# Kernel tuning notes

Hardware: AMD Instinct MI355X
Metric: run time of the kernel (lower is better)

## Reference

```python
import jax, jax.numpy as jnp
import numpy as np

TOP_K = 2
LOGIT_SCALE = 1.0


def setup_inputs() -> dict:
    key = jax.random.key(0)
    k = jax.random.split(key, 5)
    B, S, C = 1, 1024, 1024
    E, I = 8, 1024           # experts, per-expert intermediate
    x = jax.random.normal(k[0], (B, S, C), dtype=jnp.float32)
    router_w = jax.random.normal(k[1], (E, C), dtype=jnp.float32) * 0.02
    w_in = jax.random.normal(k[2], (E, 2 * I, C), dtype=jnp.float32) * 0.02
    b_in = jnp.zeros((E, 2 * I), dtype=jnp.float32)
    w_out = jax.random.normal(k[3], (E, C, I), dtype=jnp.float32) * 0.02
    b_out = jnp.zeros((E, C), dtype=jnp.float32)
    return {"x": x, "router_w": router_w, "w_in": w_in, "b_in": b_in,
            "w_out": w_out, "b_out": b_out}


def reference(x, router_w, w_in, b_in, w_out, b_out):
    B, S, C = x.shape
    E = router_w.shape[0]
    xt = x.reshape(-1, C)                               # [T, C] flattened tokens
    T = xt.shape[0]

    # Router: softmax over all experts, then top-k probs as combine weights.
    logits = (xt @ router_w.T) * LOGIT_SCALE            # [T, E]
    probs = jax.nn.softmax(logits, axis=-1)
    top_w, top_idx = jax.lax.top_k(probs, TOP_K)        # [T, K]

    # Sparse gate matrix: nonzero only at the top-k experts per token.
    gate = jnp.zeros((T, E), dtype=probs.dtype)
    gate = gate.at[jnp.arange(T)[:, None], top_idx].set(top_w)  # [T, E]

    # Expert SwiGLU MLP, dense over experts, masked combine by gate.
    h = jnp.einsum('tc,eoc->teo', xt, w_in) + b_in      # [T, E, 2I]
    g, u = jnp.split(h, 2, axis=-1)                     # gate / input halves
    a = jax.nn.silu(g) * u                              # swiglu  [T, E, I]
    y = jnp.einsum('tei,eci->tec', a, w_out) + b_out    # [T, E, C]
    out = jnp.einsum('te,tec->tc', gate, y)             # combine top-k experts
    return out.reshape(B, S, C)
```

## Files before the change

kernel.cpp:

```cpp
#include <hip/hip_runtime.h>
#include <hip/hip_bf16.h>
#include <stdint.h>

#define TTOK 1024
#define CDIM 1024
#define NEXP 8
#define IDIM 1024
#define TWOI 2048
#define NSLOT 2048

typedef float f32x4 __attribute__((ext_vector_type(4)));
typedef short s16x8 __attribute__((ext_vector_type(8)));
typedef unsigned short u16;
typedef u16 u16x4 __attribute__((ext_vector_type(4)));
typedef u16 u16x8 __attribute__((ext_vector_type(8)));

__device__ __forceinline__ u16 f2bf(float f) {
  unsigned x = __float_as_uint(f);
  x += 0x7fffu + ((x >> 16) & 1u);
  return (u16)(x >> 16);
}

__device__ __forceinline__ void gload_lds16(const void* g, void* l) {
  __builtin_amdgcn_global_load_lds(
      (const __attribute__((address_space(1))) void*)g,
      (__attribute__((address_space(3))) void*)l, 16, 0, 0);
}

__global__ __launch_bounds__(64) void router_k(const float* __restrict__ x,
                                               const float* __restrict__ rw,
                                               float* __restrict__ topw,
                                               int* __restrict__ topidx,
                                               u16* __restrict__ xb) {
  const int t = blockIdx.x;
  const int lane = threadIdx.x;
  float p[NEXP];
#pragma unroll
  for (int e = 0; e < NEXP; ++e) p[e] = 0.f;
  const float* xr = x + (size_t)t * CDIM;
  u16* xbr = xb + (size_t)t * CDIM;
  for (int c0 = lane * 4; c0 < CDIM; c0 += 64 * 4) {
    f32x4 xv = *(const f32x4*)(xr + c0);
    u16x4 xc;
#pragma unroll
    for (int q = 0; q < 4; ++q) xc[q] = f2bf(xv[q]);
    *(u16x4*)(xbr + c0) = xc;
#pragma unroll
    for (int e = 0; e < NEXP; ++e) {
      f32x4 wv = *(const f32x4*)(rw + (size_t)e * CDIM + c0);
      p[e] += xv[0] * wv[0] + xv[1] * wv[1] + xv[2] * wv[2] + xv[3] * wv[3];
    }
  }
#pragma unroll
  for (int e = 0; e < NEXP; ++e) {
    float v = p[e];
#pragma unroll
    for (int off = 32; off >= 1; off >>= 1) v += __shfl_xor(v, off);
    p[e] = v;
  }
  if (lane == 0) {
    float m = p[0];
#pragma unroll
    for (int e = 1; e < NEXP; ++e) m = fmaxf(m, p[e]);
    float pe[NEXP];
    float den = 0.f;
#pragma unroll
    for (int e = 0; e < NEXP; ++e) { pe[e] = __expf(p[e] - m); den += pe[e]; }
    int i0 = 0;
#pragma unroll
    for (int e = 1; e < NEXP; ++e) if (p[e] > p[i0]) i0 = e;
    int i1 = (i0 == 0) ? 1 : 0;
#pragma unroll
    for (int e = 0; e < NEXP; ++e) if (e != i0 && p[e] > p[i1]) i1 = e;
    const float inv = 1.f / den;
    topw[t * 2] = pe[i0] * inv;
    topw[t * 2 + 1] = pe[i1] * inv;
    topidx[t * 2] = i0;
    topidx[t * 2 + 1] = i1;
  }
}

__global__ __launch_bounds__(1024) void build_k(const int* __restrict__ topidx,
                                                int* __restrict__ meta,
                                                int* __restrict__ slot_token,
                                                int* __restrict__ slot_expert,
                                                int* __restrict__ tok2slot) {
  __shared__ int cnt[NEXP], off[NEXP], cur[NEXP];
  const int t = threadIdx.x;
  if (t < NEXP) { cnt[t] = 0; cur[t] = 0; }
  __syncthreads();
  const int e0 = topidx[t * 2];
  const int e1 = topidx[t * 2 + 1];
  atomicAdd(&cnt[e0], 1);
  atomicAdd(&cnt[e1], 1);
  __syncthreads();
  if (t == 0) {
    int acc = 0;
    for (int e = 0; e < NEXP; ++e) { off[e] = acc; acc += cnt[e]; }
  }
  __syncthreads();
  if (t < NEXP) { meta[t] = cnt[t]; meta[16 + t] = off[t]; }
  {
    const int p0 = atomicAdd(&cur[e0], 1);
    const int s0 = off[e0] + p0;
    slot_token[s0] = t;
    slot_expert[s0] = e0;
    tok2slot[t * 2] = s0;
    const int p1 = atomicAdd(&cur[e1], 1);
    const int s1 = off[e1] + p1;
    slot_token[s1] = t;
    slot_expert[s1] = e1;
    tok2slot[t * 2 + 1] = s1;
  }
}

template <int BM, bool GATHER, bool BIAS>
__global__ __launch_bounds__(256) void gemm_k(const u16* __restrict__ A,
                                              const float* __restrict__ W,
                                              float* __restrict__ O,
                                              const float* __restrict__ bias,
                                              const int* __restrict__ meta,
                                              const int* __restrict__ slot_token,
                                              int N, int K) {
  constexpr int BN = 64;
  constexpr int WM = BM / 2;
  constexpr int WN = BN / 2;
  constexpr int MR = WM / 16;
  constexpr int NR = WN / 16;
  constexpr int AG = BM / 32;

  const int e = blockIdx.z;
  const int cnt = meta[e];
  const int m0 = blockIdx.y * BM;
  if (m0 >= cnt) return;
  const int off = meta[16 + e];
  const int n0 = blockIdx.x * BN;

  __shared__ u16 sA[2][BM * 64];
  __shared__ u16 sB[2][BN * 64];

  const int tid = threadIdx.x;
  const int lane = tid & 63;
  const int w = tid >> 6;
  const int wr = w >> 1;
  const int wc = w & 1;

  const u16* aSrc[AG];
#pragma unroll
  for (int i = 0; i < AG; ++i) {
    const int r = w * (BM / 4) + i * 8 + (lane >> 3);
    int rr = m0 + r;
    if (rr > cnt - 1) rr = cnt - 1;
    const int rowg = GATHER ? slot_token[off + rr] : (off + rr);
    const int cs = (lane & 7) ^ (r & 7);
    aSrc[i] = A + (size_t)rowg * K + cs * 8;
  }
  int aDst[AG];
#pragma unroll
  for (int i = 0; i < AG; ++i) aDst[i] = (w * (BM / 4) + i * 8) * 64 + lane * 8;

  const int brow = tid >> 2;
  const int bq = tid & 3;
  const float* bSrc = W + ((size_t)e * N + (n0 + brow)) * K + bq * 16;
  const int brow7 = brow & 7;
  const int bOff0 = brow * 64 + (((bq * 2) ^ brow7) * 8);
  const int bOff1 = brow * 64 + (((bq * 2 + 1) ^ brow7) * 8);

  f32x4 acc[MR][NR];
#pragma unroll
  for (int m = 0; m < MR; ++m)
#pragma unroll
    for (int n = 0; n < NR; ++n) acc[m][n] = (f32x4){0.f, 0.f, 0.f, 0.f};

  {
#pragma unroll
    for (int i = 0; i < AG; ++i) gload_lds16(aSrc[i], &sA[0][aDst[i]]);
    f32x4 v0 = *(const f32x4*)(bSrc);
    f32x4 v1 = *(const f32x4*)(bSrc + 4);
    f32x4 v2 = *(const f32x4*)(bSrc + 8);
    f32x4 v3 = *(const f32x4*)(bSrc + 12);
    u16x8 lo, hi;
#pragma unroll
    for (int q = 0; q < 4; ++q) lo[q] = f2bf(v0[q]);
#pragma unroll
    for (int q = 0; q < 4; ++q) lo[4 + q] = f2bf(v1[q]);
#pragma unroll
    for (int q = 0; q < 4; ++q) hi[q] = f2bf(v2[q]);
#pragma unroll
    for (int q = 0; q < 4; ++q) hi[4 + q] = f2bf(v3[q]);
    *(u16x8*)(&sB[0][bOff0]) = lo;
    *(u16x8*)(&sB[0][bOff1]) = hi;
  }
  __syncthreads();

  int c = 0;
  for (int k0 = 0; k0 < K; k0 += 64) {
    const int nk = k0 + 64;
    const bool has_next = nk < K;

    f32x4 v0, v1, v2, v3;
    if (has_next) {
#pragma unroll
      for (int i = 0; i < AG; ++i) gload_lds16(aSrc[i] + nk, &sA[1 - c][aDst[i]]);
      const float* bs = bSrc + nk;
      v0 = *(const f32x4*)(bs);
      v1 = *(const f32x4*)(bs + 4);
      v2 = *(const f32x4*)(bs + 8);
      v3 = *(const f32x4*)(bs + 12);
    }

#pragma unroll
    for (int kh = 0; kh < 2; ++kh) {
      const int j = kh * 4 + (lane >> 4);
      s16x8 af[MR], bf[NR];
#pragma unroll
      for (int m = 0; m < MR; ++m) {
        const int r = wr * WM + m * 16 + (lane & 15);
        af[m] = *(const s16x8*)(&sA[c][r * 64 + ((j ^ (r & 7)) * 8)]);
      }
#pragma unroll
      for (int n = 0; n < NR; ++n) {
        const int r = wc * WN + n * 16 + (lane & 15);
        bf[n] = *(const s16x8*)(&sB[c][r * 64 + ((j ^ (r & 7)) * 8)]);
      }
#pragma unroll
      for (int m = 0; m < MR; ++m)
#pragma unroll
        for (int n = 0; n < NR; ++n)
          acc[m][n] = __builtin_amdgcn_mfma_f32_16x16x32_bf16(af[m], bf[n], acc[m][n], 0, 0, 0);
    }

    if (has_next) {
      u16x8 lo, hi;
#pragma unroll
      for (int q = 0; q < 4; ++q) lo[q] = f2bf(v0[q]);
#pragma unroll
      for (int q = 0; q < 4; ++q) lo[4 + q] = f2bf(v1[q]);
#pragma unroll
      for (int q = 0; q < 4; ++q) hi[q] = f2bf(v2[q]);
#pragma unroll
      for (int q = 0; q < 4; ++q) hi[4 + q] = f2bf(v3[q]);
      *(u16x8*)(&sB[1 - c][bOff0]) = lo;
      *(u16x8*)(&sB[1 - c][bOff1]) = hi;
    }

    __syncthreads();
    c ^= 1;
  }

#pragma unroll
  for (int m = 0; m < MR; ++m) {
#pragma unroll
    for (int jj = 0; jj < 4; ++jj) {
      const int tr = wr * WM + m * 16 + ((lane >> 4) * 4) + jj;
      if (m0 + tr < cnt) {
        const size_t slot = (size_t)(off + m0 + tr);
#pragma unroll
        for (int n = 0; n < NR; ++n) {
          const int col = n0 + wc * WN + n * 16 + (lane & 15);
          float v = acc[m][n][jj];
          if (BIAS) v += bias[(size_t)e * N + col];
          O[slot * N + col] = v;
        }
      }
    }
  }
}

__global__ __launch_bounds__(256) void swiglu_k(const float* __restrict__ h,
                                                const float* __restrict__ b_in,
                                                const int* __restrict__ slot_expert,
                                                u16* __restrict__ a) {
  const int s = blockIdx.x;
  const int e = slot_expert[s];
  const int i = threadIdx.x * 4;
  f32x4 g = *(const f32x4*)(h + (size_t)s * TWOI + i);
  f32x4 u = *(const f32x4*)(h + (size_t)s * TWOI + IDIM + i);
  f32x4 bg = *(const f32x4*)(b_in + (size_t)e * TWOI + i);
  f32x4 bu = *(const f32x4*)(b_in + (size_t)e * TWOI + IDIM + i);
  u16x4 o;
#pragma unroll
  for (int q = 0; q < 4; ++q) {
    const float gg = g[q] + bg[q];
    const float uu = u[q] + bu[q];
    const float sv = gg / (1.f + __expf(-gg));
    o[q] = f2bf(sv * uu);
  }
  *(u16x4*)(a + (size_t)s * IDIM + i) = o;
}

__global__ __launch_bounds__(256) void combine_k(const float* __restrict__ y,
                                                 const float* __restrict__ topw,
                                                 const int* __restrict__ tok2slot,
                                                 float* __restrict__ out) {
  const int idx = blockIdx.x * 256 + threadIdx.x;
  const int t = idx >> 8;
  const int c4 = (idx & 255) * 4;
  const int s0 = tok2slot[t * 2];
  const int s1 = tok2slot[t * 2 + 1];
  const float w0 = topw[t * 2];
  const float w1 = topw[t * 2 + 1];
  f32x4 y0 = *(const f32x4*)(y + (size_t)s0 * CDIM + c4);
  f32x4 y1 = *(const f32x4*)(y + (size_t)s1 * CDIM + c4);
  f32x4 o;
#pragma unroll
  for (int q = 0; q < 4; ++q) o[q] = w0 * y0[q] + w1 * y1[q];
  *(f32x4*)(out + (size_t)t * CDIM + c4) = o;
}

extern "C" void kernel_launch(void* const* d_in, const int* in_sizes, int n_in,
                              void* d_out, int out_size, void* d_ws, size_t ws_size,
                              hipStream_t stream) {
  const float* x = (const float*)d_in[0];
  const float* rw = (const float*)d_in[1];
  const float* w_in = (const float*)d_in[2];
  const float* b_in = (const float*)d_in[3];
  const float* w_out = (const float*)d_in[4];
  const float* b_out = (const float*)d_in[5];
  float* out = (float*)d_out;
  char* ws = (char*)d_ws;

  int* meta = (int*)ws;
  int* slot_token = (int*)(ws + 1024);
  int* slot_expert = (int*)(ws + 1024 + 8192);
  int* tok2slot = (int*)(ws + 1024 + 16384);
  float* topw = (float*)(ws + 1024 + 24576);
  int* topidx = (int*)(ws + 1024 + 32768);
  u16* xb = (u16*)(ws + 65536);
  float* h = (float*)(ws + 65536 + (2u << 20));
  u16* a = (u16*)(ws + 65536 + (18u << 20));
  float* y = (float*)(ws + 65536 + (22u << 20));

  router_k<<<TTOK, 64, 0, stream>>>(x, rw, topw, topidx, xb);
  build_k<<<1, 1024, 0, stream>>>(topidx, meta, slot_token, slot_expert, tok2slot);
  gemm_k<128, true, false><<<dim3(32, 16, NEXP), 256, 0, stream>>>(
      xb, w_in, h, nullptr, meta, slot_token, TWOI, CDIM);
  swiglu_k<<<NSLOT, 256, 0, stream>>>(h, b_in, slot_expert, a);
  gemm_k<64, false, true><<<dim3(16, 32, NEXP), 256, 0, stream>>>(
      a, w_out, y, b_out, meta, slot_token, CDIM, IDIM);
  combine_k<<<1024, 256, 0, stream>>>(y, topw, tok2slot, out);
}
```

Before: 197.9 us.

## Fuse SwiGLU into first GEMM epilogue and combine into second via atomics

The first expert GEMM now interleaves gate and up rows of w_in so each tile holds matching g/u columns. It applies bias and SwiGLU in its epilogue via a lane shuffle and writes bf16 activations directly, which removes the fp32 h buffer and the separate swiglu kernel. The second GEMM scales by the gate weight and atomically adds into a zeroed output, which removes the y buffer and the combine kernel. In exchange it adds a memset, float atomics with nondeterministic summation order, and a smaller BM=64 tile for GEMM1 that rereads the weights more often.

```diff
diff --git a/kernel.cpp b/kernel.cpp
--- a/kernel.cpp
+++ b/kernel.cpp
@@ -81,10 +81,10 @@
 }
 
 __global__ __launch_bounds__(1024) void build_k(const int* __restrict__ topidx,
+                                                const float* __restrict__ topw,
                                                 int* __restrict__ meta,
                                                 int* __restrict__ slot_token,
-                                                int* __restrict__ slot_expert,
-                                                int* __restrict__ tok2slot) {
+                                                float* __restrict__ gatew) {
   __shared__ int cnt[NEXP], off[NEXP], cur[NEXP];
   const int t = threadIdx.x;
   if (t < NEXP) { cnt[t] = 0; cur[t] = 0; }
@@ -104,40 +104,30 @@
     const int p0 = atomicAdd(&cur[e0], 1);
     const int s0 = off[e0] + p0;
     slot_token[s0] = t;
-    slot_expert[s0] = e0;
-    tok2slot[t * 2] = s0;
+    gatew[s0] = topw[t * 2];
     const int p1 = atomicAdd(&cur[e1], 1);
     const int s1 = off[e1] + p1;
     slot_token[s1] = t;
-    slot_expert[s1] = e1;
-    tok2slot[t * 2 + 1] = s1;
-  }
-}
-
-template <int BM, bool GATHER, bool BIAS>
-__global__ __launch_bounds__(256) void gemm_k(const u16* __restrict__ A,
-                                              const float* __restrict__ W,
-                                              float* __restrict__ O,
-                                              const float* __restrict__ bias,
-                                              const int* __restrict__ meta,
-                                              const int* __restrict__ slot_token,
-                                              int N, int K) {
-  constexpr int BN = 64;
-  constexpr int WM = BM / 2;
-  constexpr int WN = BN / 2;
-  constexpr int MR = WM / 16;
-  constexpr int NR = WN / 16;
-  constexpr int AG = BM / 32;
-
+    gatew[s1] = topw[t * 2 + 1];
+  }
+}
+
+__global__ __launch_bounds__(256) void gemm1_k(const u16* __restrict__ A,
+                                               const float* __restrict__ W,
+                                               const float* __restrict__ b_in,
+                                               u16* __restrict__ Aout,
+                                               const int* __restrict__ meta,
+                                               const int* __restrict__ slot_token) {
+  constexpr int BM = 64, K = CDIM;
   const int e = blockIdx.z;
   const int cnt = meta[e];
   const int m0 = blockIdx.y * BM;
   if (m0 >= cnt) return;
   const int off = meta[16 + e];
-  const int n0 = blockIdx.x * BN;
+  const int i0 = blockIdx.x * 32;
 
   __shared__ u16 sA[2][BM * 64];
-  __shared__ u16 sB[2][BN * 64];
+  __shared__ u16 sB[2][64 * 64];
 
   const int tid = threadIdx.x;
   const int lane = tid & 63;
@@ -145,36 +135,36 @@
   const int wr = w >> 1;
   const int wc = w & 1;
 
-  const u16* aSrc[AG];
-#pragma unroll
-  for (int i = 0; i < AG; ++i) {
-    const int r = w * (BM / 4) + i * 8 + (lane >> 3);
+  const u16* aSrc[2];
+  int aDst[2];
+#pragma unroll
+  for (int i = 0; i < 2; ++i) {
+    const int r = w * 16 + i * 8 + (lane >> 3);
     int rr = m0 + r;
     if (rr > cnt - 1) rr = cnt - 1;
-    const int rowg = GATHER ? slot_token[off + rr] : (off + rr);
+    const int rowg = slot_token[off + rr];
     const int cs = (lane & 7) ^ (r & 7);
     aSrc[i] = A + (size_t)rowg * K + cs * 8;
-  }
-  int aDst[AG];
-#pragma unroll
-  for (int i = 0; i < AG; ++i) aDst[i] = (w * (BM / 4) + i * 8) * 64 + lane * 8;
+    aDst[i] = (w * 16 + i * 8) * 64 + lane * 8;
+  }
 
   const int brow = tid >> 2;
   const int bq = tid & 3;
-  const float* bSrc = W + ((size_t)e * N + (n0 + brow)) * K + bq * 16;
+  const int wrow = (brow & 1) ? (IDIM + i0 + (brow >> 1)) : (i0 + (brow >> 1));
+  const float* bSrc = W + ((size_t)e * TWOI + wrow) * K + bq * 16;
   const int brow7 = brow & 7;
   const int bOff0 = brow * 64 + (((bq * 2) ^ brow7) * 8);
   const int bOff1 = brow * 64 + (((bq * 2 + 1) ^ brow7) * 8);
 
-  f32x4 acc[MR][NR];
-#pragma unroll
-  for (int m = 0; m < MR; ++m)
-#pragma unroll
-    for (int n = 0; n < NR; ++n) acc[m][n] = (f32x4){0.f, 0.f, 0.f, 0.f};
+  f32x4 acc[2][2];
+#pragma unroll
+  for (int m = 0; m < 2; ++m)
+#pragma unroll
+    for (int n = 0; n < 2; ++n) acc[m][n] = (f32x4){0.f, 0.f, 0.f, 0.f};
 
   {
 #pragma unroll
-    for (int i = 0; i < AG; ++i) gload_lds16(aSrc[i], &sA[0][aDst[i]]);
+    for (int i = 0; i < 2; ++i) gload_lds16(aSrc[i], &sA[0][aDst[i]]);
     f32x4 v0 = *(const f32x4*)(bSrc);
     f32x4 v1 = *(const f32x4*)(bSrc + 4);
     f32x4 v2 = *(const f32x4*)(bSrc + 8);
@@ -197,39 +187,36 @@
   for (int k0 = 0; k0 < K; k0 += 64) {
     const int nk = k0 + 64;
     const bool has_next = nk < K;
-
     f32x4 v0, v1, v2, v3;
     if (has_next) {
 #pragma unroll
-      for (int i = 0; i < AG; ++i) gload_lds16(aSrc[i] + nk, &sA[1 - c][aDst[i]]);
+      for (int i = 0; i < 2; ++i) gload_lds16(aSrc[i] + nk, &sA[1 - c][aDst[i]]);
       const float* bs = bSrc + nk;
       v0 = *(const f32x4*)(bs);
       v1 = *(const f32x4*)(bs + 4);
       v2 = *(const f32x4*)(bs + 8);
       v3 = *(const f32x4*)(bs + 12);
     }
-
 #pragma unroll
     for (int kh = 0; kh < 2; ++kh) {
       const int j = kh * 4 + (lane >> 4);
-      s16x8 af[MR], bf[NR];
-#pragma unroll
-      for (int m = 0; m < MR; ++m) {
-        const int r = wr * WM + m * 16 + (lane & 15);
+      s16x8 af[2], bf[2];
+#pragma unroll
+      for (int m = 0; m < 2; ++m) {
+        const int r = wr * 32 + m * 16 + (lane & 15);
         af[m] = *(const s16x8*)(&sA[c][r * 64 + ((j ^ (r & 7)) * 8)]);
       }
 #pragma unroll
-      for (int n = 0; n < NR; ++n) {
-        const int r = wc * WN + n * 16 + (lane & 15);
+      for (int n = 0; n < 2; ++n) {
+        const int r = wc * 32 + n * 16 + (lane & 15);
         bf[n] = *(const s16x8*)(&sB[c][r * 64 + ((j ^ (r & 7)) * 8)]);
       }
 #pragma unroll
-      for (int m = 0; m < MR; ++m)
-#pragma unroll
-        for (int n = 0; n < NR; ++n)
+      for (int m = 0; m < 2; ++m)
+#pragma unroll
+        for (int n = 0; n < 2; ++n)
           acc[m][n] = __builtin_amdgcn_mfma_f32_16x16x32_bf16(af[m], bf[n], acc[m][n], 0, 0, 0);
     }
-
     if (has_next) {
       u16x8 lo, hi;
 #pragma unroll
@@ -243,69 +230,172 @@
       *(u16x8*)(&sB[1 - c][bOff0]) = lo;
       *(u16x8*)(&sB[1 - c][bOff1]) = hi;
     }
-
     __syncthreads();
     c ^= 1;
   }
 
 #pragma unroll
-  for (int m = 0; m < MR; ++m) {
+  for (int m = 0; m < 2; ++m) {
 #pragma unroll
     for (int jj = 0; jj < 4; ++jj) {
-      const int tr = wr * WM + m * 16 + ((lane >> 4) * 4) + jj;
+      const int tr = wr * 32 + m * 16 + ((lane >> 4) * 4) + jj;
+      const bool live = (m0 + tr) < cnt;
+      const size_t slot = (size_t)(off + m0 + tr);
+#pragma unroll
+      for (int n = 0; n < 2; ++n) {
+        const int cc = wc * 32 + n * 16 + (lane & 15);
+        const int wrow_c = (cc & 1) ? (IDIM + i0 + (cc >> 1)) : (i0 + (cc >> 1));
+        float v = acc[m][n][jj] + b_in[(size_t)e * TWOI + wrow_c];
+        const float vo = __shfl_xor(v, 1);
+        if (!(lane & 1) && live) {
+          const float g = v, u = vo;
+          const float aval = (g / (1.f + __expf(-g))) * u;
+          Aout[slot * IDIM + i0 + (cc >> 1)] = f2bf(aval);
+        }
+      }
+    }
+  }
+}
+
+__global__ __launch_bounds__(256) void gemm2_k(const u16* __restrict__ A,
+                                               const float* __restrict__ W,
+                                               const float* __restrict__ b_out,
+                                               float* __restrict__ out,
+                                               const int* __restrict__ meta,
+                                               const int* __restrict__ slot_token,
+                                               const float* __restrict__ gatew) {
+  constexpr int BM = 64, K = IDIM;
+  const int e = blockIdx.z;
+  const int cnt = meta[e];
+  const int m0 = blockIdx.y * BM;
+  if (m0 >= cnt) return;
+  const int off = meta[16 + e];
+  const int n0 = blockIdx.x * 64;
+
+  __shared__ u16 sA[2][BM * 64];
+  __shared__ u16 sB[2][64 * 64];
+
+  const int tid = threadIdx.x;
+  const int lane = tid & 63;
+  const int w = tid >> 6;
+  const int wr = w >> 1;
+  const int wc = w & 1;
+
+  const u16* aSrc[2];
+  int aDst[2];
+#pragma unroll
+  for (int i = 0; i < 2; ++i) {
+    const int r = w * 16 + i * 8 + (lane >> 3);
+    int rr = m0 + r;
+    if (rr > cnt - 1) rr = cnt - 1;
+    const int cs = (lane & 7) ^ (r & 7);
+    aSrc[i] = A + (size_t)(off + rr) * K + cs * 8;
+    aDst[i] = (w * 16 + i * 8) * 64 + lane * 8;
+  }
+
+  const int brow = tid >> 2;
+  const int bq = tid & 3;
+  const float* bSrc = W + ((size_t)e * CDIM + (n0 + brow)) * K + bq * 16;
+  const int brow7 = brow & 7;
+  const int bOff0 = brow * 64 + (((bq * 2) ^ brow7) * 8);
+  const int bOff1 = brow * 64 + (((bq * 2 + 1) ^ brow7) * 8);
+
+  f32x4 acc[2][2];
+#pragma unroll
+  for (int m = 0; m < 2; ++m)
+#pragma unroll
+    for (int n = 0; n < 2; ++n) acc[m][n] = (f32x4){0.f, 0.f, 0.f, 0.f};
+
+  {
+#pragma unroll
+    for (int i = 0; i < 2; ++i) gload_lds16(aSrc[i], &sA[0][aDst[i]]);
+    f32x4 v0 = *(const f32x4*)(bSrc);
+    f32x4 v1 = *(const f32x4*)(bSrc + 4);
+    f32x4 v2 = *(const f32x4*)(bSrc + 8);
+    f32x4 v3 = *(const f32x4*)(bSrc + 12);
+    u16x8 lo, hi;
+#pragma unroll
+    for (int q = 0; q < 4; ++q) lo[q] = f2bf(v0[q]);
+#pragma unroll
+    for (int q = 0; q < 4; ++q) lo[4 + q] = f2bf(v1[q]);
+#pragma unroll
+    for (int q = 0; q < 4; ++q) hi[q] = f2bf(v2[q]);
+#pragma unroll
+    for (int q = 0; q < 4; ++q) hi[4 + q] = f2bf(v3[q]);
+    *(u16x8*)(&sB[0][bOff0]) = lo;
+    *(u16x8*)(&sB[0][bOff1]) = hi;
+  }
+  __syncthreads();
+
+  int c = 0;
+  for (int k0 = 0; k0 < K; k0 += 64) {
+    const int nk = k0 + 64;
+    const bool has_next = nk < K;
+    f32x4 v0, v1, v2, v3;
+    if (has_next) {
+#pragma unroll
+      for (int i = 0; i < 2; ++i) gload_lds16(aSrc[i] + nk, &sA[1 - c][aDst[i]]);
+      const float* bs = bSrc + nk;
+      v0 = *(const f32x4*)(bs);
+      v1 = *(const f32x4*)(bs + 4);
+      v2 = *(const f32x4*)(bs + 8);
+      v3 = *(const f32x4*)(bs + 12);
+    }
+#pragma unroll
+    for (int kh = 0; kh < 2; ++kh) {
+      const int j = kh * 4 + (lane >> 4);
+      s16x8 af[2], bf[2];
+#pragma unroll
+      for (int m = 0; m < 2; ++m) {
+        const int r = wr * 32 + m * 16 + (lane & 15);
+        af[m] = *(const s16x8*)(&sA[c][r * 64 + ((j ^ (r & 7)) * 8)]);
+      }
+#pragma unroll
+      for (int n = 0; n < 2; ++n) {
+        const int r = wc * 32 + n * 16 + (lane & 15);
+        bf[n] = *(const s16x8*)(&sB[c][r * 64 + ((j ^ (r & 7)) * 8)]);
+      }
+#pragma unroll
+      for (int m = 0; m < 2; ++m)
+#pragma unroll
+        for (int n = 0; n < 2; ++n)
+          acc[m][n] = __builtin_amdgcn_mfma_f32_16x16x32_bf16(af[m], bf[n], acc[m][n], 0, 0, 0);
+    }
+    if (has_next) {
+      u16x8 lo, hi;
+#pragma unroll
+      for (int q = 0; q < 4; ++q) lo[q] = f2bf(v0[q]);
+#pragma unroll
+      for (int q = 0; q < 4; ++q) lo[4 + q] = f2bf(v1[q]);
+#pragma unroll
+      for (int q = 0; q < 4; ++q) hi[q] = f2bf(v2[q]);
+#pragma unroll
+      for (int q = 0; q < 4; ++q) hi[4 + q] = f2bf(v3[q]);
+      *(u16x8*)(&sB[1 - c][bOff0]) = lo;
+      *(u16x8*)(&sB[1 - c][bOff1]) = hi;
+    }
+    __syncthreads();
+    c ^= 1;
+  }
+
+#pragma unroll
+  for (int m = 0; m < 2; ++m) {
+#pragma unroll
+    for (int jj = 0; jj < 4; ++jj) {
+      const int tr = wr * 32 + m * 16 + ((lane >> 4) * 4) + jj;
       if (m0 + tr < cnt) {
-        const size_t slot = (size_t)(off + m0 + tr);
-#pragma unroll
-        for (int n = 0; n < NR; ++n) {
-          const int col = n0 + wc * WN + n * 16 + (lane & 15);
-          float v = acc[m][n][jj];
-          if (BIAS) v += bias[(size_t)e * N + col];
-          O[slot * N + col] = v;
+        const int slot = off + m0 + tr;
+        const int tok = slot_token[slot];
+        const float gw = gatew[slot];
+#pragma unroll
+        for (int n = 0; n < 2; ++n) {
+          const int col = n0 + wc * 32 + n * 16 + (lane & 15);
+          const float v = acc[m][n][jj] + b_out[(size_t)e * CDIM + col];
+          atomicAdd(&out[(size_t)tok * CDIM + col], gw * v);
         }
       }
     }
   }
-}
-
-__global__ __launch_bounds__(256) void swiglu_k(const float* __restrict__ h,
-                                                const float* __restrict__ b_in,
-                                                const int* __restrict__ slot_expert,
-                                                u16* __restrict__ a) {
-  const int s = blockIdx.x;
-  const int e = slot_expert[s];
-  const int i = threadIdx.x * 4;
-  f32x4 g = *(const f32x4*)(h + (size_t)s * TWOI + i);
-  f32x4 u = *(const f32x4*)(h + (size_t)s * TWOI + IDIM + i);
-  f32x4 bg = *(const f32x4*)(b_in + (size_t)e * TWOI + i);
-  f32x4 bu = *(const f32x4*)(b_in + (size_t)e * TWOI + IDIM + i);
-  u16x4 o;
-#pragma unroll
-  for (int q = 0; q < 4; ++q) {
-    const float gg = g[q] + bg[q];
-    const float uu = u[q] + bu[q];
-    const float sv = gg / (1.f + __expf(-gg));
-    o[q] = f2bf(sv * uu);
-  }
-  *(u16x4*)(a + (size_t)s * IDIM + i) = o;
-}
-
-__global__ __launch_bounds__(256) void combine_k(const float* __restrict__ y,
-                                                 const float* __restrict__ topw,
-                                                 const int* __restrict__ tok2slot,
-                                                 float* __restrict__ out) {
-  const int idx = blockIdx.x * 256 + threadIdx.x;
-  const int t = idx >> 8;
-  const int c4 = (idx & 255) * 4;
-  const int s0 = tok2slot[t * 2];
-  const int s1 = tok2slot[t * 2 + 1];
-  const float w0 = topw[t * 2];
-  const float w1 = topw[t * 2 + 1];
-  f32x4 y0 = *(const f32x4*)(y + (size_t)s0 * CDIM + c4);
-  f32x4 y1 = *(const f32x4*)(y + (size_t)s1 * CDIM + c4);
-  f32x4 o;
-#pragma unroll
-  for (int q = 0; q < 4; ++q) o[q] = w0 * y0[q] + w1 * y1[q];
-  *(f32x4*)(out + (size_t)t * CDIM + c4) = o;
 }
 
 extern "C" void kernel_launch(void* const* d_in, const int* in_sizes, int n_in,
@@ -322,21 +412,17 @@
 
   int* meta = (int*)ws;
   int* slot_token = (int*)(ws + 1024);
-  int* slot_expert = (int*)(ws + 1024 + 8192);
-  int* tok2slot = (int*)(ws + 1024 + 16384);
-  float* topw = (float*)(ws + 1024 + 24576);
-  int* topidx = (int*)(ws + 1024 + 32768);
+  float* topw = (float*)(ws + 1024 + 8192);
+  int* topidx = (int*)(ws + 1024 + 16384);
+  float* gatew = (float*)(ws + 1024 + 24576);
   u16* xb = (u16*)(ws + 65536);
-  float* h = (float*)(ws + 65536 + (2u << 20));
-  u16* a = (u16*)(ws + 65536 + (18u << 20));
-  float* y = (float*)(ws + 65536 + (22u << 20));
-
+  u16* a = (u16*)(ws + 65536 + (2u << 20));
+
+  hipMemsetAsync(out, 0, (size_t)TTOK * CDIM * sizeof(float), stream);
   router_k<<<TTOK, 64, 0, stream>>>(x, rw, topw, topidx, xb);
-  build_k<<<1, 1024, 0, stream>>>(topidx, meta, slot_token, slot_expert, tok2slot);
-  gemm_k<128, true, false><<<dim3(32, 16, NEXP), 256, 0, stream>>>(
-      xb, w_in, h, nullptr, meta, slot_token, TWOI, CDIM);
-  swiglu_k<<<NSLOT, 256, 0, stream>>>(h, b_in, slot_expert, a);
-  gemm_k<64, false, true><<<dim3(16, 32, NEXP), 256, 0, stream>>>(
-      a, w_out, y, b_out, meta, slot_token, CDIM, IDIM);
-  combine_k<<<1024, 256, 0, stream>>>(y, topw, tok2slot, out);
-}
+  build_k<<<1, 1024, 0, stream>>>(topidx, topw, meta, slot_token, gatew);
+  gemm1_k<<<dim3(32, 32, NEXP), 256, 0, stream>>>(
+      xb, w_in, b_in, a, meta, slot_token);
+  gemm2_k<<<dim3(16, 32, NEXP), 256, 0, stream>>>(
+      a, w_out, b_out, out, meta, slot_token, gatew);
+}
```

Result: slower. 203.1 us (+2.6%).
